# Performance work log

Hardware: AMD Instinct MI355X
Metric: run time of the kernel (lower is better)

The kernel has to match this reference:

```python
import jax, jax.numpy as jnp
import numpy as np

T = 10          # time_steps
IN_DIM = 784    # 28*28
HID = 256
NCLS = 47
THRESH = 1.0
TAU_MEM = 2.0   # LIF membrane time constant
TAU_OUT = 2.0   # readout EMA time constant


@jax.custom_vjp
def spike_fn(u):
    # Heaviside spike on (v - threshold), surrogate gradient in bwd.
    return (u >= 0.0).astype(u.dtype)

def _spike_fwd(u):
    return spike_fn(u), u

def _spike_bwd(u, g):
    # sigmoid surrogate derivative, slope 4
    s = jax.nn.sigmoid(4.0 * u)
    return (g * 4.0 * s * (1.0 - s),)

spike_fn.defvjp(_spike_fwd, _spike_bwd)


def setup_inputs() -> dict:
    key = jax.random.key(0)
    k1, k2, k3 = jax.random.split(key, 3)
    x = jax.random.uniform(k1, (4096, 1, 28, 28), dtype=jnp.float32)
    W1 = jax.random.normal(k2, (IN_DIM, HID), dtype=jnp.float32) / np.float32(np.sqrt(IN_DIM))
    b1 = jnp.zeros((HID,), jnp.float32)
    Wr = jax.random.normal(k3, (HID, NCLS), dtype=jnp.float32) / np.float32(np.sqrt(HID))
    br = jnp.zeros((NCLS,), jnp.float32)
    return {"x": x, "W1": W1, "b1": b1, "Wr": Wr, "br": br}


def reference(x, W1, b1, Wr, br):
    B = x.shape[0]
    xf = x.reshape(B, -1)  # [B, 784] pixel intensities in [0,1]
    # rate_encode_flat: Bernoulli(p=pixel) spikes per timestep -> [T, B, 784]
    ek = jax.random.key(42)
    seq = (jax.random.uniform(ek, (T, B, IN_DIM), dtype=xf.dtype) < xf[None]).astype(xf.dtype)

    def step(carry, s_t):
        v_hid, v_out = carry
        I_hid = s_t @ W1 + b1                      # [B, HID]
        v_hid = v_hid + (I_hid - v_hid) / TAU_MEM  # leaky integration
        spk = spike_fn(v_hid - THRESH)             # spike emission
        v_hid = v_hid * (1.0 - spk)                # hard reset to 0
        I = spk @ Wr + br                          # [B, NCLS]
        v_out = v_out + (I - v_out) / TAU_OUT      # output EMA
        return (v_hid, v_out), None

    init = (jnp.zeros((B, HID), xf.dtype), jnp.zeros((B, NCLS), xf.dtype))
    (_, v_out), _ = jax.lax.scan(step, init, seq)
    return v_out
```

## Files before the change

### kernel.cpp

```cpp
#include <hip/hip_runtime.h>
#include <stdint.h>


#define T_STEPS 10
#define BATCH   4096
#define IN_DIM  784
#define HID     256
#define NCLS    47
#define NROWS   (T_STEPS * BATCH)
#define KWORDS  25
#define KPAD    800

#define WS_IALL_OFF 0u
#define WS_W1HI_OFF 46039040u
#define WS_W1MD_OFF (46039040u + 409600u)
#define WS_W1LO_OFF (46039040u + 819200u)

typedef __attribute__((ext_vector_type(8))) short    bf16x8;
typedef __attribute__((ext_vector_type(4))) float    f32x4;
typedef __attribute__((ext_vector_type(4))) uint32_t u32x4;

#define TF_G1(x0, x1) \
    "v_add_u32 " x0 ", " x0 ", " x1 "\n\t" \
    "v_alignbit_b32 " x1 ", " x1 ", " x1 ", 19\n\t" \
    "v_xor_b32 " x1 ", " x1 ", " x0 "\n\t" \
    "v_add_u32 " x0 ", " x0 ", " x1 "\n\t" \
    "v_alignbit_b32 " x1 ", " x1 ", " x1 ", 17\n\t" \
    "v_xor_b32 " x1 ", " x1 ", " x0 "\n\t" \
    "v_add_u32 " x0 ", " x0 ", " x1 "\n\t" \
    "v_alignbit_b32 " x1 ", " x1 ", " x1 ", 6\n\t" \
    "v_xor_b32 " x1 ", " x1 ", " x0 "\n\t" \
    "v_add_u32 " x0 ", " x0 ", " x1 "\n\t" \
    "v_alignbit_b32 " x1 ", " x1 ", " x1 ", 26\n\t" \
    "v_xor_b32 " x1 ", " x1 ", " x0 "\n\t"

#define TF_G2(x0, x1) \
    "v_add_u32 " x0 ", " x0 ", " x1 "\n\t" \
    "v_alignbit_b32 " x1 ", " x1 ", " x1 ", 15\n\t" \
    "v_xor_b32 " x1 ", " x1 ", " x0 "\n\t" \
    "v_add_u32 " x0 ", " x0 ", " x1 "\n\t" \
    "v_alignbit_b32 " x1 ", " x1 ", " x1 ", 3\n\t" \
    "v_xor_b32 " x1 ", " x1 ", " x0 "\n\t" \
    "v_add_u32 " x0 ", " x0 ", " x1 "\n\t" \
    "v_alignbit_b32 " x1 ", " x1 ", " x1 ", 16\n\t" \
    "v_xor_b32 " x1 ", " x1 ", " x0 "\n\t" \
    "v_add_u32 " x0 ", " x0 ", " x1 "\n\t" \
    "v_alignbit_b32 " x1 ", " x1 ", " x1 ", 8\n\t" \
    "v_xor_b32 " x1 ", " x1 ", " x0 "\n\t"

#define TF_HASH9(m, ib, J42) do {                                   \
    uint32_t _x0, _x1;                                              \
    asm("v_add_u32 %1, " J42 ", %2\n\t"         \
        "v_mov_b32 %0, %1\n\t"                  \
        "v_alignbit_b32 %1, %1, %1, 19\n\t"                         \
        "v_xor_b32 %1, %1, %0\n\t"                                  \
        "v_add_u32 %0, %0, %1\n\t"                          \
        "v_alignbit_b32 %1, %1, %1, 17\n\t"                         \
        "v_xor_b32 %1, %1, %0\n\t"                                  \
        "v_add_u32 %0, %0, %1\n\t"                          \
        "v_alignbit_b32 %1, %1, %1, 6\n\t"                          \
        "v_xor_b32 %1, %1, %0\n\t"                                  \
        "v_add_u32 %0, %0, %1\n\t"                          \
        "v_alignbit_b32 %1, %1, %1, 26\n\t"                         \
        "v_xor_b32 %1, %1, %0\n\t"                                  \
        "v_add_u32 %0, 42, %0\n\t"                   \
        "v_add_u32 %1, 0x1bd11bf1, %1\n\t"         \
        TF_G2("%0", "%1")                                \
        "v_add_u32 %0, 0x1bd11bf0, %0\n\t"           \
        "v_add_u32 %1, 2, %1\n\t"                  \
        TF_G1("%0", "%1")                               \
        "v_add_u32 %1, 45, %1\n\t"                 \
        TF_G2("%0", "%1")                              \
        "v_add_u32 %0, 42, %0\n\t"                   \
        "v_add_u32 %1, 0x1bd11bf4, %1\n\t"         \
        TF_G1("%0", "%1")                              \
        "v_add_u32 %0, 0x1bd11bf0, %0\n\t"           \
        "v_add_u32 %1, 5, %1\n\t"                  \
        "v_xor_b32 %0, %0, %1\n\t"                       \
        "v_lshrrev_b32 %0, 9, %0"                          \
        : "=&v"(_x0), "=&v"(_x1) : "v"(ib));                        \
    m = _x0;                                                        \
} while (0)

__global__ __launch_bounds__(256) void splitk_k(
        const float* __restrict__ W1, ushort* __restrict__ hiT,
        ushort* __restrict__ midT, ushort* __restrict__ loT) {
    int n = blockIdx.x;
    for (int k = threadIdx.x; k < KPAD; k += 256) {
        float w = (k < IN_DIM) ? W1[k * HID + n] : 0.0f;
        uint32_t u = __float_as_uint(w);
        uint32_t hb = (u + 0x7FFFu + ((u >> 16) & 1u)) >> 16;
        float hf = __uint_as_float(hb << 16);
        float r1 = w - hf;
        uint32_t u1 = __float_as_uint(r1);
        uint32_t mb = (u1 + 0x7FFFu + ((u1 >> 16) & 1u)) >> 16;
        float mf2 = __uint_as_float(mb << 16);
        float r2 = r1 - mf2;
        uint32_t u2 = __float_as_uint(r2);
        uint32_t lb = (u2 + 0x7FFFu + ((u2 >> 16) & 1u)) >> 16;
        hiT [n * KPAD + k] = (ushort)hb;
        midT[n * KPAD + k] = (ushort)mb;
        loT [n * KPAD + k] = (ushort)lb;
    }
}

#define LDS_A  0
#define LDS_BH 4096
#define LDS_BM 20480
#define LDS_BL 36864

__global__ __launch_bounds__(256, 3) void fused_gemm_k(
        const ushort* __restrict__ hiT, const ushort* __restrict__ midT,
        const ushort* __restrict__ loT, const float* __restrict__ b1,
        const float* __restrict__ x, float* __restrict__ I_all) {
    __shared__ __align__(16) char lds[53248];

    const int tid = threadIdx.x;
    const int l   = tid & 63;
    const int wv  = tid >> 6;
    const int t   = blockIdx.x >> 6;
    const int b0  = (blockIdx.x & 63) << 6;
    const int m0  = blockIdx.x << 6;

    f32x4 acc[4][4] = {};

    const int q   = l >> 4;
    const int sig = q ^ (l & 3) ^ ((l >> 2) & 3);
    const int a_base = LDS_A + ((l & 15) << 6) + (sig << 4);
    const int b_off  = (((wv << 6) + (l & 15)) << 6) + (sig << 4);

    const ushort* hi_p[4];
    const ushort* md_p[4];
    const ushort* lo_p[4];
    int ldst_c[4];
#pragma unroll
    for (int i = 0; i < 4; ++i) {
        int s  = (wv << 8) + (i << 6) + l;
        int n  = s >> 2;
        int qs = s & 3;
        int qd = qs ^ (n & 3) ^ ((n >> 2) & 3);
        size_t eoff = (size_t)n * KPAD + ((size_t)qd << 3);
        hi_p[i] = hiT  + eoff;
        md_p[i] = midT + eoff;
        lo_p[i] = loT  + eoff;
        ldst_c[i] = ((wv << 8) + (i << 6)) << 4;
    }

    const int er = tid >> 2;
    const int eq = tid & 3;
    const int ea = LDS_A + (er << 6) + ((eq ^ (er & 3) ^ ((er >> 2) & 3)) << 4);
    const int row_b = b0 + er;
    const float* xp = x + (size_t)row_b * IN_DIM + (eq << 3);
    uint32_t ib = (uint32_t)(row_b * IN_DIM) + (uint32_t)(eq << 3)
                + (uint32_t)t * (uint32_t)(BATCH * IN_DIM);

    for (int kw = 0; kw < KWORDS; ++kw) {
        __syncthreads();

#pragma unroll
        for (int i = 0; i < 4; ++i) {
            __builtin_amdgcn_global_load_lds(
                (const __attribute__((address_space(1))) void*)hi_p[i],
                (__attribute__((address_space(3))) void*)(lds + LDS_BH + ldst_c[i]),
                16, 0, 0);
            __builtin_amdgcn_global_load_lds(
                (const __attribute__((address_space(1))) void*)md_p[i],
                (__attribute__((address_space(3))) void*)(lds + LDS_BM + ldst_c[i]),
                16, 0, 0);
            __builtin_amdgcn_global_load_lds(
                (const __attribute__((address_space(1))) void*)lo_p[i],
                (__attribute__((address_space(3))) void*)(lds + LDS_BL + ldst_c[i]),
                16, 0, 0);
            hi_p[i] += 32;  md_p[i] += 32;  lo_p[i] += 32;
        }

        {
            u32x4 v = {0u, 0u, 0u, 0u};
            if (!(kw == 24 && eq >= 2)) {
                float4 xa = *(const float4*)xp;
                float4 xb = *(const float4*)(xp + 4);
                uint32_t m0h, m1h, m2h, m3h, m4h, m5h, m6h, m7h;
                TF_HASH9(m0h, ib, "42");
                TF_HASH9(m1h, ib, "43");
                TF_HASH9(m2h, ib, "44");
                TF_HASH9(m3h, ib, "45");
                TF_HASH9(m4h, ib, "46");
                TF_HASH9(m5h, ib, "47");
                TF_HASH9(m6h, ib, "48");
                TF_HASH9(m7h, ib, "49");
                uint32_t c0 = ((float)m0h < xa.x * 8388608.0f) ? 0x3F80u : 0u;
                uint32_t c1 = ((float)m1h < xa.y * 8388608.0f) ? 0x3F800000u : 0u;
                uint32_t c2 = ((float)m2h < xa.z * 8388608.0f) ? 0x3F80u : 0u;
                uint32_t c3 = ((float)m3h < xa.w * 8388608.0f) ? 0x3F800000u : 0u;
                uint32_t c4 = ((float)m4h < xb.x * 8388608.0f) ? 0x3F80u : 0u;
                uint32_t c5 = ((float)m5h < xb.y * 8388608.0f) ? 0x3F800000u : 0u;
                uint32_t c6 = ((float)m6h < xb.z * 8388608.0f) ? 0x3F80u : 0u;
                uint32_t c7 = ((float)m7h < xb.w * 8388608.0f) ? 0x3F800000u : 0u;
                v.x = c0 | c1;  v.y = c2 | c3;  v.z = c4 | c5;  v.w = c6 | c7;
            }
            *(u32x4*)(lds + ea) = v;
        }
        xp += 32;  ib += 32u;

        __syncthreads();

        bf16x8 af[4];
#pragma unroll
        for (int mt = 0; mt < 4; ++mt)
            af[mt] = *(const bf16x8*)(lds + a_base + (mt << 10));
#pragma unroll
        for (int nt = 0; nt < 4; ++nt) {
            bf16x8 bh = *(const bf16x8*)(lds + LDS_BH + b_off + (nt << 10));
            bf16x8 bm = *(const bf16x8*)(lds + LDS_BM + b_off + (nt << 10));
            bf16x8 bl = *(const bf16x8*)(lds + LDS_BL + b_off + (nt << 10));
#pragma unroll
            for (int mt = 0; mt < 4; ++mt) {
                acc[mt][nt] = __builtin_amdgcn_mfma_f32_16x16x32_bf16(af[mt], bh, acc[mt][nt], 0, 0, 0);
                acc[mt][nt] = __builtin_amdgcn_mfma_f32_16x16x32_bf16(af[mt], bm, acc[mt][nt], 0, 0, 0);
                acc[mt][nt] = __builtin_amdgcn_mfma_f32_16x16x32_bf16(af[mt], bl, acc[mt][nt], 0, 0, 0);
            }
        }
    }

    const int c0 = l & 15;
    float b1v[4];
#pragma unroll
    for (int nt = 0; nt < 4; ++nt)
        b1v[nt] = b1[(wv << 6) + (nt << 4) + c0];
#pragma unroll
    for (int mt = 0; mt < 4; ++mt) {
#pragma unroll
        for (int nt = 0; nt < 4; ++nt) {
            int col = (wv << 6) + (nt << 4) + c0;
#pragma unroll
            for (int r = 0; r < 4; ++r) {
                int row = m0 + (mt << 4) + (q << 2) + r;
                I_all[(size_t)row * HID + col] = acc[mt][nt][r] + b1v[nt];
            }
        }
    }
}

__global__ __launch_bounds__(256) void scanout_k(
        const float* __restrict__ I_all, const float* __restrict__ Wr,
        const float* __restrict__ br, float* __restrict__ out) {
    __shared__ float gl[16 * 256];
    const int tid = threadIdx.x;
    const int b0  = blockIdx.x << 4;

#pragma unroll 4
    for (int b = 0; b < 16; ++b) {
        const float* p = I_all + ((size_t)(b0 + b) << 8) + tid;
        float v = 0.f, ga = 0.f, wt = 0.0009765625f;
#pragma unroll
        for (int t = 0; t < T_STEPS; ++t) {
            float I = p[(size_t)t * BATCH * HID];
            v = v + (I - v) * 0.5f;
            if (v >= 1.0f) { ga += wt; v = 0.f; }
            wt += wt;
        }
        gl[(b << 8) + tid] = ga;
    }
    __syncthreads();

    const int wv = tid >> 6;
    const int c  = tid & 63;
    if (c >= NCLS) return;
    float acc[4] = {0.f, 0.f, 0.f, 0.f};
    for (int h4 = 0; h4 < 64; ++h4) {
        float w0 = Wr[((h4 << 2) + 0) * NCLS + c];
        float w1 = Wr[((h4 << 2) + 1) * NCLS + c];
        float w2 = Wr[((h4 << 2) + 2) * NCLS + c];
        float w3 = Wr[((h4 << 2) + 3) * NCLS + c];
#pragma unroll
        for (int j = 0; j < 4; ++j) {
            float4 gg = *(float4*)&gl[(((wv << 2) + j) << 8) + (h4 << 2)];
            acc[j] = fmaf(gg.x, w0, acc[j]);
            acc[j] = fmaf(gg.y, w1, acc[j]);
            acc[j] = fmaf(gg.z, w2, acc[j]);
            acc[j] = fmaf(gg.w, w3, acc[j]);
        }
    }
    float brv = br[c] * 0.9990234375f;
#pragma unroll
    for (int j = 0; j < 4; ++j)
        out[(b0 + (wv << 2) + j) * NCLS + c] = acc[j] + brv;
}

extern "C" void kernel_launch(void* const* d_in, const int* in_sizes, int n_in,
                              void* d_out, int out_size, void* d_ws, size_t ws_size,
                              hipStream_t stream) {
    const float* x  = (const float*)d_in[0];
    const float* W1 = (const float*)d_in[1];
    const float* b1 = (const float*)d_in[2];
    const float* Wr = (const float*)d_in[3];
    const float* br = (const float*)d_in[4];
    float* out = (float*)d_out;

    float*  I_all = (float*) ((char*)d_ws + WS_IALL_OFF);
    ushort* w1hi  = (ushort*)((char*)d_ws + WS_W1HI_OFF);
    ushort* w1md  = (ushort*)((char*)d_ws + WS_W1MD_OFF);
    ushort* w1lo  = (ushort*)((char*)d_ws + WS_W1LO_OFF);

    splitk_k<<<HID, 256, 0, stream>>>(W1, w1hi, w1md, w1lo);
    fused_gemm_k<<<NROWS / 64, 256, 0, stream>>>(w1hi, w1md, w1lo, b1, x, I_all);
    scanout_k<<<BATCH / 16, 256, 0, stream>>>(I_all, Wr, br, out);
}
```

Measured before the change: 198.7 us.

## Precompute bit-packed spikes in separate kernel and split GEMM N across blocks

Moves the Threefry Bernoulli spike generation out of the GEMM into a dedicated kernel that writes bit-packed spike words, fused with the W1 bf16 triple split. Previously each of the N-split duplicates would hash inputs, so splitting the GEMM over two column halves (128 cols per block, 1280 blocks, smaller LDS, higher occupancy bound) is now possible without redundant hashing. The GEMM then expands one byte per thread into bf16 ones/zeros. This adds an extra kernel pass and spike buffer traffic in exchange for less compute in the GEMM inner loop and better parallelism.

```diff
diff --git a/kernel.cpp b/kernel.cpp
--- a/kernel.cpp
+++ b/kernel.cpp
@@ -12,6 +12,7 @@
 #define KPAD    800
 
 #define WS_IALL_OFF 0u
+#define WS_SPK_OFF  41943040u
 #define WS_W1HI_OFF 46039040u
 #define WS_W1MD_OFF (46039040u + 409600u)
 #define WS_W1LO_OFF (46039040u + 819200u)
@@ -82,125 +83,148 @@
     m = _x0;                                                        \
 } while (0)
 
-__global__ __launch_bounds__(256) void splitk_k(
+#define SPIKE8(wrd, ib, xa, xb, base_bit) do {                             \
+    uint32_t m0h, m1h, m2h, m3h, m4h, m5h, m6h, m7h;                       \
+    TF_HASH9(m0h, (ib), "42");  TF_HASH9(m1h, (ib), "43");                 \
+    TF_HASH9(m2h, (ib), "44");  TF_HASH9(m3h, (ib), "45");                 \
+    TF_HASH9(m4h, (ib), "46");  TF_HASH9(m5h, (ib), "47");                 \
+    TF_HASH9(m6h, (ib), "48");  TF_HASH9(m7h, (ib), "49");                 \
+    if ((float)m0h < (xa).x * 8388608.0f) wrd |= (1u << ((base_bit) + 0)); \
+    if ((float)m1h < (xa).y * 8388608.0f) wrd |= (1u << ((base_bit) + 1)); \
+    if ((float)m2h < (xa).z * 8388608.0f) wrd |= (1u << ((base_bit) + 2)); \
+    if ((float)m3h < (xa).w * 8388608.0f) wrd |= (1u << ((base_bit) + 3)); \
+    if ((float)m4h < (xb).x * 8388608.0f) wrd |= (1u << ((base_bit) + 4)); \
+    if ((float)m5h < (xb).y * 8388608.0f) wrd |= (1u << ((base_bit) + 5)); \
+    if ((float)m6h < (xb).z * 8388608.0f) wrd |= (1u << ((base_bit) + 6)); \
+    if ((float)m7h < (xb).w * 8388608.0f) wrd |= (1u << ((base_bit) + 7)); \
+} while (0)
+
+__global__ __launch_bounds__(256) void spike_split_k(
+        const float* __restrict__ x, uint32_t* __restrict__ spk,
         const float* __restrict__ W1, ushort* __restrict__ hiT,
         ushort* __restrict__ midT, ushort* __restrict__ loT) {
-    int n = blockIdx.x;
-    for (int k = threadIdx.x; k < KPAD; k += 256) {
-        float w = (k < IN_DIM) ? W1[k * HID + n] : 0.0f;
-        uint32_t u = __float_as_uint(w);
-        uint32_t hb = (u + 0x7FFFu + ((u >> 16) & 1u)) >> 16;
-        float hf = __uint_as_float(hb << 16);
-        float r1 = w - hf;
-        uint32_t u1 = __float_as_uint(r1);
-        uint32_t mb = (u1 + 0x7FFFu + ((u1 >> 16) & 1u)) >> 16;
-        float mf2 = __uint_as_float(mb << 16);
-        float r2 = r1 - mf2;
-        uint32_t u2 = __float_as_uint(r2);
-        uint32_t lb = (u2 + 0x7FFFu + ((u2 >> 16) & 1u)) >> 16;
-        hiT [n * KPAD + k] = (ushort)hb;
-        midT[n * KPAD + k] = (ushort)mb;
-        loT [n * KPAD + k] = (ushort)lb;
-    }
+    const int tid = threadIdx.x;
+
+    if (blockIdx.x >= 2000) {
+        int n = blockIdx.x - 2000;
+        for (int k = tid; k < KPAD; k += 256) {
+            float w = (k < IN_DIM) ? W1[k * HID + n] : 0.0f;
+            uint32_t u = __float_as_uint(w);
+            uint32_t hb = (u + 0x7FFFu + ((u >> 16) & 1u)) >> 16;
+            float hf = __uint_as_float(hb << 16);
+            float r1 = w - hf;
+            uint32_t u1 = __float_as_uint(r1);
+            uint32_t mb = (u1 + 0x7FFFu + ((u1 >> 16) & 1u)) >> 16;
+            float mf2 = __uint_as_float(mb << 16);
+            float r2 = r1 - mf2;
+            uint32_t u2 = __float_as_uint(r2);
+            uint32_t lb = (u2 + 0x7FFFu + ((u2 >> 16) & 1u)) >> 16;
+            hiT [n * KPAD + k] = (ushort)hb;
+            midT[n * KPAD + k] = (ushort)mb;
+            loT [n * KPAD + k] = (ushort)lb;
+        }
+        return;
+    }
+
+    const int bid = blockIdx.x;
+    const int kw  = bid / 80;
+    const int rem = bid - kw * 80;
+    const int tg  = rem >> 4;
+    const int b   = ((rem & 15) << 8) + tid;
+    const int t0  = tg << 1;
+    const int kbase = kw << 5;
+
+    const uint32_t tstep = (uint32_t)(BATCH * IN_DIM);
+    const uint32_t i0 = (uint32_t)(b * IN_DIM + kbase) + (uint32_t)t0 * tstep;
+    const float* xr = x + b * IN_DIM + kbase;
+
+    uint32_t w0 = 0u, w1 = 0u;
+    const int ng = (kw == 24) ? 2 : 4;
+
+    for (int g = 0; g < ng; ++g) {
+        float4 xa = *(const float4*)&xr[g << 3];
+        float4 xb = *(const float4*)&xr[(g << 3) + 4];
+        uint32_t ib0 = i0 + (uint32_t)(g << 3);
+        uint32_t ib1 = ib0 + tstep;
+        switch (g) {
+            case 0: SPIKE8(w0, ib0, xa, xb, 0);  SPIKE8(w1, ib1, xa, xb, 0);  break;
+            case 1: SPIKE8(w0, ib0, xa, xb, 8);  SPIKE8(w1, ib1, xa, xb, 8);  break;
+            case 2: SPIKE8(w0, ib0, xa, xb, 16); SPIKE8(w1, ib1, xa, xb, 16); break;
+            default:SPIKE8(w0, ib0, xa, xb, 24); SPIKE8(w1, ib1, xa, xb, 24); break;
+        }
+    }
+    spk[(kw * T_STEPS + t0    ) * BATCH + b] = w0;
+    spk[(kw * T_STEPS + t0 + 1) * BATCH + b] = w1;
 }
 
 #define LDS_A  0
 #define LDS_BH 4096
-#define LDS_BM 20480
-#define LDS_BL 36864
-
-__global__ __launch_bounds__(256, 3) void fused_gemm_k(
+#define LDS_BM 12288
+#define LDS_BL 20480
+
+__global__ __launch_bounds__(256, 5) void gemm_mfma_k(
         const ushort* __restrict__ hiT, const ushort* __restrict__ midT,
         const ushort* __restrict__ loT, const float* __restrict__ b1,
-        const float* __restrict__ x, float* __restrict__ I_all) {
-    __shared__ __align__(16) char lds[53248];
+        const uint32_t* __restrict__ spk, float* __restrict__ I_all) {
+    __shared__ __align__(16) char lds[28672];
 
     const int tid = threadIdx.x;
     const int l   = tid & 63;
     const int wv  = tid >> 6;
-    const int t   = blockIdx.x >> 6;
-    const int b0  = (blockIdx.x & 63) << 6;
-    const int m0  = blockIdx.x << 6;
-
-    f32x4 acc[4][4] = {};
+    const int bid = blockIdx.x;
+    const int t    = bid >> 7;
+    const int rem  = bid & 127;
+    const int b0   = (rem >> 1) << 6;
+    const int nc0  = (rem & 1) << 7;
+    const int m0   = (t << 12) + b0;
+
+    f32x4 acc[4][2] = {};
 
     const int q   = l >> 4;
     const int sig = q ^ (l & 3) ^ ((l >> 2) & 3);
     const int a_base = LDS_A + ((l & 15) << 6) + (sig << 4);
-    const int b_off  = (((wv << 6) + (l & 15)) << 6) + (sig << 4);
-
-    const ushort* hi_p[4];
-    const ushort* md_p[4];
-    const ushort* lo_p[4];
-    int ldst_c[4];
-#pragma unroll
-    for (int i = 0; i < 4; ++i) {
-        int s  = (wv << 8) + (i << 6) + l;
-        int n  = s >> 2;
-        int qs = s & 3;
-        int qd = qs ^ (n & 3) ^ ((n >> 2) & 3);
-        size_t eoff = (size_t)n * KPAD + ((size_t)qd << 3);
-        hi_p[i] = hiT  + eoff;
-        md_p[i] = midT + eoff;
-        lo_p[i] = loT  + eoff;
-        ldst_c[i] = ((wv << 8) + (i << 6)) << 4;
-    }
+    const int b_base = (((wv << 5) + (l & 15)) << 6) + (sig << 4);
 
     const int er = tid >> 2;
     const int eq = tid & 3;
     const int ea = LDS_A + (er << 6) + ((eq ^ (er & 3) ^ ((er >> 2) & 3)) << 4);
-    const int row_b = b0 + er;
-    const float* xp = x + (size_t)row_b * IN_DIM + (eq << 3);
-    uint32_t ib = (uint32_t)(row_b * IN_DIM) + (uint32_t)(eq << 3)
-                + (uint32_t)t * (uint32_t)(BATCH * IN_DIM);
+    const uint32_t* wptr = spk + (size_t)t * BATCH + b0 + er;
 
     for (int kw = 0; kw < KWORDS; ++kw) {
         __syncthreads();
 
 #pragma unroll
-        for (int i = 0; i < 4; ++i) {
+        for (int i = 0; i < 2; ++i) {
+            int s  = (i << 8) + tid;
+            int n  = s >> 2;
+            int qs = s & 3;
+            int qd = qs ^ (n & 3) ^ ((n >> 2) & 3);
+            size_t gb = (size_t)(nc0 + n) * (KPAD * 2) + ((size_t)kw << 6) + ((size_t)qd << 4);
+            int ldst = s << 4;
             __builtin_amdgcn_global_load_lds(
-                (const __attribute__((address_space(1))) void*)hi_p[i],
-                (__attribute__((address_space(3))) void*)(lds + LDS_BH + ldst_c[i]),
+                (const __attribute__((address_space(1))) void*)((const char*)hiT + gb),
+                (__attribute__((address_space(3))) void*)(lds + LDS_BH + ldst),
                 16, 0, 0);
             __builtin_amdgcn_global_load_lds(
-                (const __attribute__((address_space(1))) void*)md_p[i],
-                (__attribute__((address_space(3))) void*)(lds + LDS_BM + ldst_c[i]),
+                (const __attribute__((address_space(1))) void*)((const char*)midT + gb),
+                (__attribute__((address_space(3))) void*)(lds + LDS_BM + ldst),
                 16, 0, 0);
             __builtin_amdgcn_global_load_lds(
-                (const __attribute__((address_space(1))) void*)lo_p[i],
-                (__attribute__((address_space(3))) void*)(lds + LDS_BL + ldst_c[i]),
+                (const __attribute__((address_space(1))) void*)((const char*)loT + gb),
+                (__attribute__((address_space(3))) void*)(lds + LDS_BL + ldst),
                 16, 0, 0);
-            hi_p[i] += 32;  md_p[i] += 32;  lo_p[i] += 32;
         }
 
         {
-            u32x4 v = {0u, 0u, 0u, 0u};
-            if (!(kw == 24 && eq >= 2)) {
-                float4 xa = *(const float4*)xp;
-                float4 xb = *(const float4*)(xp + 4);
-                uint32_t m0h, m1h, m2h, m3h, m4h, m5h, m6h, m7h;
-                TF_HASH9(m0h, ib, "42");
-                TF_HASH9(m1h, ib, "43");
-                TF_HASH9(m2h, ib, "44");
-                TF_HASH9(m3h, ib, "45");
-                TF_HASH9(m4h, ib, "46");
-                TF_HASH9(m5h, ib, "47");
-                TF_HASH9(m6h, ib, "48");
-                TF_HASH9(m7h, ib, "49");
-                uint32_t c0 = ((float)m0h < xa.x * 8388608.0f) ? 0x3F80u : 0u;
-                uint32_t c1 = ((float)m1h < xa.y * 8388608.0f) ? 0x3F800000u : 0u;
-                uint32_t c2 = ((float)m2h < xa.z * 8388608.0f) ? 0x3F80u : 0u;
-                uint32_t c3 = ((float)m3h < xa.w * 8388608.0f) ? 0x3F800000u : 0u;
-                uint32_t c4 = ((float)m4h < xb.x * 8388608.0f) ? 0x3F80u : 0u;
-                uint32_t c5 = ((float)m5h < xb.y * 8388608.0f) ? 0x3F800000u : 0u;
-                uint32_t c6 = ((float)m6h < xb.z * 8388608.0f) ? 0x3F80u : 0u;
-                uint32_t c7 = ((float)m7h < xb.w * 8388608.0f) ? 0x3F800000u : 0u;
-                v.x = c0 | c1;  v.y = c2 | c3;  v.z = c4 | c5;  v.w = c6 | c7;
-            }
+            uint32_t w = wptr[(size_t)kw * NROWS];
+            uint32_t byte = (w >> (eq << 3)) & 0xFFu;
+            u32x4 v;
+            v.x = ((byte &   1u) ? 0x3F80u : 0u) | ((byte &   2u) ? 0x3F800000u : 0u);
+            v.y = ((byte &   4u) ? 0x3F80u : 0u) | ((byte &   8u) ? 0x3F800000u : 0u);
+            v.z = ((byte &  16u) ? 0x3F80u : 0u) | ((byte &  32u) ? 0x3F800000u : 0u);
+            v.w = ((byte &  64u) ? 0x3F80u : 0u) | ((byte & 128u) ? 0x3F800000u : 0u);
             *(u32x4*)(lds + ea) = v;
         }
-        xp += 32;  ib += 32u;
 
         __syncthreads();
 
@@ -209,10 +233,10 @@
         for (int mt = 0; mt < 4; ++mt)
             af[mt] = *(const bf16x8*)(lds + a_base + (mt << 10));
 #pragma unroll
-        for (int nt = 0; nt < 4; ++nt) {
-            bf16x8 bh = *(const bf16x8*)(lds + LDS_BH + b_off + (nt << 10));
-            bf16x8 bm = *(const bf16x8*)(lds + LDS_BM + b_off + (nt << 10));
-            bf16x8 bl = *(const bf16x8*)(lds + LDS_BL + b_off + (nt << 10));
+        for (int nt = 0; nt < 2; ++nt) {
+            bf16x8 bh = *(const bf16x8*)(lds + LDS_BH + b_base + (nt << 10));
+            bf16x8 bm = *(const bf16x8*)(lds + LDS_BM + b_base + (nt << 10));
+            bf16x8 bl = *(const bf16x8*)(lds + LDS_BL + b_base + (nt << 10));
 #pragma unroll
             for (int mt = 0; mt < 4; ++mt) {
                 acc[mt][nt] = __builtin_amdgcn_mfma_f32_16x16x32_bf16(af[mt], bh, acc[mt][nt], 0, 0, 0);
@@ -223,15 +247,15 @@
     }
 
     const int c0 = l & 15;
-    float b1v[4];
-#pragma unroll
-    for (int nt = 0; nt < 4; ++nt)
-        b1v[nt] = b1[(wv << 6) + (nt << 4) + c0];
+    float b1v[2];
+#pragma unroll
+    for (int nt = 0; nt < 2; ++nt)
+        b1v[nt] = b1[nc0 + (wv << 5) + (nt << 4) + c0];
 #pragma unroll
     for (int mt = 0; mt < 4; ++mt) {
 #pragma unroll
-        for (int nt = 0; nt < 4; ++nt) {
-            int col = (wv << 6) + (nt << 4) + c0;
+        for (int nt = 0; nt < 2; ++nt) {
+            int col = nc0 + (wv << 5) + (nt << 4) + c0;
 #pragma unroll
             for (int r = 0; r < 4; ++r) {
                 int row = m0 + (mt << 4) + (q << 2) + r;
@@ -297,12 +321,13 @@
     const float* br = (const float*)d_in[4];
     float* out = (float*)d_out;
 
-    float*  I_all = (float*) ((char*)d_ws + WS_IALL_OFF);
-    ushort* w1hi  = (ushort*)((char*)d_ws + WS_W1HI_OFF);
-    ushort* w1md  = (ushort*)((char*)d_ws + WS_W1MD_OFF);
-    ushort* w1lo  = (ushort*)((char*)d_ws + WS_W1LO_OFF);
-
-    splitk_k<<<HID, 256, 0, stream>>>(W1, w1hi, w1md, w1lo);
-    fused_gemm_k<<<NROWS / 64, 256, 0, stream>>>(w1hi, w1md, w1lo, b1, x, I_all);
+    float*    I_all = (float*)   ((char*)d_ws + WS_IALL_OFF);
+    uint32_t* spk   = (uint32_t*)((char*)d_ws + WS_SPK_OFF);
+    ushort*   w1hi  = (ushort*)  ((char*)d_ws + WS_W1HI_OFF);
+    ushort*   w1md  = (ushort*)  ((char*)d_ws + WS_W1MD_OFF);
+    ushort*   w1lo  = (ushort*)  ((char*)d_ws + WS_W1LO_OFF);
+
+    spike_split_k<<<2256, 256, 0, stream>>>(x, spk, W1, w1hi, w1md, w1lo);
+    gemm_mfma_k<<<1280, 256, 0, stream>>>(w1hi, w1md, w1lo, b1, spk, I_all);
     scanout_k<<<BATCH / 16, 256, 0, stream>>>(I_all, Wr, br, out);
 }
```

Result: slower. 206.4 us (+3.8%).
